# Performance work log

Hardware: AMD Instinct MI355X
Metric: run time of the kernel (lower is better)

Reference implementation:

```python
import jax, jax.numpy as jnp
import numpy as np

B, D_IN, D_Z, N_TRIALS = 4096, 784, 128, 256
T_TEMP = 1.0  # PVAE.t


def setup_inputs() -> dict:
    key = jax.random.key(0)
    ks = jax.random.split(key, 4)
    x = jax.random.normal(ks[0], (B, D_IN), jnp.float32)
    # uniform base samples for reparameterized Exponential(rate) draws
    u = jax.random.uniform(ks[1], (N_TRIALS, B, D_Z), jnp.float32,
                           minval=1e-7, maxval=1.0 - 1e-7)
    W_enc = jax.random.normal(ks[2], (D_IN, D_Z), jnp.float32) * 0.03
    b_enc = jnp.zeros((D_Z,), jnp.float32)
    W_dec = jax.random.normal(ks[3], (D_Z, D_IN), jnp.float32) * 0.08
    b_dec = jnp.zeros((D_IN,), jnp.float32)
    prior = jnp.zeros((1, D_Z), jnp.float32)
    return {"x": x, "u": u, "W_enc": W_enc, "b_enc": b_enc,
            "W_dec": W_dec, "b_dec": b_dec, "prior": prior}


def reference(x, u, W_enc, b_enc, W_dec, b_dec, prior):
    # encoder: du = clamp(Linear(x), max=5)
    du = jnp.minimum(x @ W_enc + b_enc, 5.0)                 # [B, Z]
    # log_rate = clamp(du + clamp(prior, max=5), max=5); rate = exp(.) + 1e-6
    log_rate = jnp.minimum(du + jnp.minimum(prior, 5.0), 5.0)
    rate = jnp.exp(log_rate) + 1e-6                          # [B, Z]
    # exponential race: e ~ Exp(1) via inverse CDF, scaled by 1/rate
    e = -jnp.log1p(-u)                                       # [T, B, Z]
    times = jnp.cumsum(e / rate[None], axis=0)               # prefix sums of arrival times
    # soft indicator (training path, t = 1.0): sigmoid((1 - times) / t)
    indicator = jax.nn.sigmoid((1.0 - times) / T_TEMP)       # [T, B, Z]
    z = jnp.sum(indicator, axis=0)                           # [B, Z] soft Poisson count
    # decoder: sigmoid(Linear(z))
    y = jax.nn.sigmoid(z @ W_dec + b_dec)                    # [B, 784]
    return (du, z, y)
```

## Files before the change

kernel.cpp:

```cpp
#include <hip/hip_runtime.h>
#include <cstdint>
#include <cstddef>

#define LOG2E 1.44269504088896340736f
#define LN2   0.69314718055994530942f

__device__ __forceinline__ float fast_log2(float x) { return __builtin_amdgcn_logf(x); }
__device__ __forceinline__ float fast_exp2(float x) { return __builtin_amdgcn_exp2f(x); }
__device__ __forceinline__ float fast_rcp(float x)  { return __builtin_amdgcn_rcpf(x); }


__global__ __launch_bounds__(256) void enc_kernel(const float* __restrict__ x,
                                                  const float* __restrict__ W,
                                                  const float* __restrict__ bias,
                                                  float* __restrict__ du) {
  __shared__ float xs[16][16];
  __shared__ float ws[16][128];
  const int tid  = threadIdx.x;
  const int row0 = blockIdx.x * 16;
  const int cg   = tid & 31;
  const int rg   = tid >> 5;

  float4 a0 = {0.f, 0.f, 0.f, 0.f};
  float4 a1 = {0.f, 0.f, 0.f, 0.f};

  for (int k0 = 0; k0 < 784; k0 += 16) {
    __syncthreads();
    if (tid < 64) {
      int r = tid >> 2, kc = (tid & 3) * 4;
      *(float4*)&xs[r][kc] = *(const float4*)&x[(size_t)(row0 + r) * 784 + k0 + kc];
    }
#pragma unroll
    for (int j = 0; j < 2; j++) {
      int i = tid + 256 * j;
      int k = i >> 5, c4 = (i & 31) * 4;
      *(float4*)&ws[k][c4] = *(const float4*)&W[(size_t)(k0 + k) * 128 + c4];
    }
    __syncthreads();
#pragma unroll
    for (int k = 0; k < 16; k++) {
      float x0 = xs[rg * 2][k];
      float x1 = xs[rg * 2 + 1][k];
      float4 w = *(const float4*)&ws[k][cg * 4];
      a0.x = fmaf(x0, w.x, a0.x); a0.y = fmaf(x0, w.y, a0.y);
      a0.z = fmaf(x0, w.z, a0.z); a0.w = fmaf(x0, w.w, a0.w);
      a1.x = fmaf(x1, w.x, a1.x); a1.y = fmaf(x1, w.y, a1.y);
      a1.z = fmaf(x1, w.z, a1.z); a1.w = fmaf(x1, w.w, a1.w);
    }
  }

  float4 bb = *(const float4*)&bias[cg * 4];
  float4 r0, r1;
  r0.x = fminf(a0.x + bb.x, 5.f); r0.y = fminf(a0.y + bb.y, 5.f);
  r0.z = fminf(a0.z + bb.z, 5.f); r0.w = fminf(a0.w + bb.w, 5.f);
  r1.x = fminf(a1.x + bb.x, 5.f); r1.y = fminf(a1.y + bb.y, 5.f);
  r1.z = fminf(a1.z + bb.z, 5.f); r1.w = fminf(a1.w + bb.w, 5.f);
  *(float4*)&du[(size_t)(row0 + rg * 2)     * 128 + cg * 4] = r0;
  *(float4*)&du[(size_t)(row0 + rg * 2 + 1) * 128 + cg * 4] = r1;
}

__global__ __launch_bounds__(256) void race_kernel(const float* __restrict__ u,
                                                   const float* __restrict__ du,
                                                   const float* __restrict__ prior,
                                                   float* __restrict__ zout) {
  const int g  = blockIdx.x * 256 + threadIdx.x;
  const int b  = g >> 6;
  const int z0 = (g & 63) * 2;

  const float2 d = *(const float2*)&du[(size_t)b * 128 + z0];
  const float2 p = *(const float2*)&prior[z0];
  const float lr0 = fminf(d.x + fminf(p.x, 5.f), 5.f);
  const float lr1 = fminf(d.y + fminf(p.y, 5.f), 5.f);
  const float rate0 = fast_exp2(lr0 * LOG2E) + 1e-6f;
  const float rate1 = fast_exp2(lr1 * LOG2E) + 1e-6f;
  const float sinv0 = -LN2 / rate0;
  const float sinv1 = -LN2 / rate1;

  float t0 = 0.f, t1 = 0.f, acc0 = 0.f, acc1 = 0.f;
  const float* up = u + (size_t)b * 128 + z0;

#pragma unroll 4
  for (int t = 0; t < 256; t++) {
    float2 uu = *(const float2*)&up[(size_t)t * (4096 * 128)];
    float l0 = fast_log2(1.f - uu.x);
    float l1 = fast_log2(1.f - uu.y);
    t0 = fmaf(l0, sinv0, t0);
    t1 = fmaf(l1, sinv1, t1);
    float e0 = fast_exp2(fmaf(t0, LOG2E, -LOG2E));
    float e1 = fast_exp2(fmaf(t1, LOG2E, -LOG2E));
    acc0 += fast_rcp(1.f + e0);
    acc1 += fast_rcp(1.f + e1);
  }
  float2 r; r.x = acc0; r.y = acc1;
  *(float2*)&zout[(size_t)b * 128 + z0] = r;
}

__global__ __launch_bounds__(256) void dec_kernel(const float* __restrict__ z,
                                                  const float* __restrict__ W,
                                                  const float* __restrict__ bias,
                                                  float* __restrict__ y) {
  __shared__ float zs[8 * 128];
  const int tid = threadIdx.x;
  const int b0  = blockIdx.x * 8;
  *(float4*)&zs[tid * 4] = *(const float4*)&z[(size_t)b0 * 128 + tid * 4];
  __syncthreads();

  for (int col = tid; col < 784; col += 256) {
    float bv = bias[col];
    float acc[8];
#pragma unroll
    for (int i = 0; i < 8; i++) acc[i] = bv;
#pragma unroll 4
    for (int k = 0; k < 128; k++) {
      float w = W[(size_t)k * 784 + col];
#pragma unroll
      for (int i = 0; i < 8; i++) acc[i] = fmaf(zs[i * 128 + k], w, acc[i]);
    }
#pragma unroll
    for (int i = 0; i < 8; i++) {
      float ex = fast_exp2(-acc[i] * LOG2E);
      y[(size_t)(b0 + i) * 784 + col] = fast_rcp(1.f + ex);
    }
  }
}

extern "C" void kernel_launch(void* const* d_in, const int* in_sizes, int n_in,
                              void* d_out, int out_size, void* d_ws, size_t ws_size,
                              hipStream_t stream) {
  const float* x     = (const float*)d_in[0];
  const float* u     = (const float*)d_in[1];
  const float* W_enc = (const float*)d_in[2];
  const float* b_enc = (const float*)d_in[3];
  const float* W_dec = (const float*)d_in[4];
  const float* b_dec = (const float*)d_in[5];
  const float* prior = (const float*)d_in[6];

  float* out = (float*)d_out;
  float* du  = out;
  float* zz  = out + 4096 * 128;
  float* y   = out + 2 * 4096 * 128;

  enc_kernel <<<256,  256, 0, stream>>>(x, W_enc, b_enc, du);
  race_kernel<<<1024, 256, 0, stream>>>(u, du, prior, zz);
  dec_kernel <<<512,  256, 0, stream>>>(zz, W_dec, b_dec, y);
}
```

Baseline: 803.9 us.

## Truncate exponential race once arrival times saturate and widen race lanes to float4

Each race thread now handles four latent dimensions with float4 loads of u, and the launch uses half as many blocks. The trial loop stops per lane once every cumulative arrival time exceeds 18, and exits the wavefront once no lane is active. This skips both the loads of u and the transcendental math for trials whose sigmoid contribution is negligible. The truncation is sound because times only increase, but it adds a small bounded error and makes runtime depend on the rate distribution. The loop also gains a wavefront vote and per-lane branch divergence.

Measured after the change: 789.1 us. No clear change (-1.8%).

```diff
diff --git a/kernel.cpp b/kernel.cpp
--- a/kernel.cpp
+++ b/kernel.cpp
@@ -64,35 +64,53 @@
                                                    const float* __restrict__ prior,
                                                    float* __restrict__ zout) {
   const int g  = blockIdx.x * 256 + threadIdx.x;
-  const int b  = g >> 6;
-  const int z0 = (g & 63) * 2;
+  const int b  = g >> 5;
+  const int z4 = (g & 31) * 4;
 
-  const float2 d = *(const float2*)&du[(size_t)b * 128 + z0];
-  const float2 p = *(const float2*)&prior[z0];
-  const float lr0 = fminf(d.x + fminf(p.x, 5.f), 5.f);
-  const float lr1 = fminf(d.y + fminf(p.y, 5.f), 5.f);
-  const float rate0 = fast_exp2(lr0 * LOG2E) + 1e-6f;
-  const float rate1 = fast_exp2(lr1 * LOG2E) + 1e-6f;
-  const float sinv0 = -LN2 / rate0;
-  const float sinv1 = -LN2 / rate1;
+  const float4 d = *(const float4*)&du[(size_t)b * 128 + z4];
+  const float4 p = *(const float4*)&prior[z4];
 
-  float t0 = 0.f, t1 = 0.f, acc0 = 0.f, acc1 = 0.f;
-  const float* up = u + (size_t)b * 128 + z0;
+  float sinv[4];
+  {
+    const float dd[4] = {d.x, d.y, d.z, d.w};
+    const float pp[4] = {p.x, p.y, p.z, p.w};
+#pragma unroll
+    for (int j = 0; j < 4; j++) {
+      float lr   = fminf(dd[j] + fminf(pp[j], 5.f), 5.f);
+      float rate = fast_exp2(lr * LOG2E) + 1e-6f;
+      sinv[j]    = -LN2 / rate;
+    }
+  }
 
-#pragma unroll 4
-  for (int t = 0; t < 256; t++) {
-    float2 uu = *(const float2*)&up[(size_t)t * (4096 * 128)];
-    float l0 = fast_log2(1.f - uu.x);
-    float l1 = fast_log2(1.f - uu.y);
-    t0 = fmaf(l0, sinv0, t0);
-    t1 = fmaf(l1, sinv1, t1);
-    float e0 = fast_exp2(fmaf(t0, LOG2E, -LOG2E));
-    float e1 = fast_exp2(fmaf(t1, LOG2E, -LOG2E));
-    acc0 += fast_rcp(1.f + e0);
-    acc1 += fast_rcp(1.f + e1);
+  float t[4]   = {0.f, 0.f, 0.f, 0.f};
+  float acc[4] = {0.f, 0.f, 0.f, 0.f};
+  const float* up = u + (size_t)b * 128 + z4;
+  const float TMAX = 18.f;
+
+  for (int tt = 0; tt < 256; tt += 2) {
+    bool act = fminf(fminf(t[0], t[1]), fminf(t[2], t[3])) < TMAX;
+    if (!__any(act)) break;
+    if (act) {
+      float4 ua = *(const float4*)&up[(size_t)tt * (4096 * 128)];
+      float4 ub = *(const float4*)&up[(size_t)(tt + 1) * (4096 * 128)];
+      const float uaj[4] = {ua.x, ua.y, ua.z, ua.w};
+      const float ubj[4] = {ub.x, ub.y, ub.z, ub.w};
+#pragma unroll
+      for (int j = 0; j < 4; j++) {
+        float l = fast_log2(1.f - uaj[j]);
+        t[j] = fmaf(l, sinv[j], t[j]);
+        float e = fast_exp2(fmaf(t[j], LOG2E, -LOG2E));
+        acc[j] += fast_rcp(1.f + e);
+        l = fast_log2(1.f - ubj[j]);
+        t[j] = fmaf(l, sinv[j], t[j]);
+        e = fast_exp2(fmaf(t[j], LOG2E, -LOG2E));
+        acc[j] += fast_rcp(1.f + e);
+      }
+    }
   }
-  float2 r; r.x = acc0; r.y = acc1;
-  *(float2*)&zout[(size_t)b * 128 + z0] = r;
+
+  float4 r; r.x = acc[0]; r.y = acc[1]; r.z = acc[2]; r.w = acc[3];
+  *(float4*)&zout[(size_t)b * 128 + z4] = r;
 }
 
 __global__ __launch_bounds__(256) void dec_kernel(const float* __restrict__ z,
@@ -140,7 +158,7 @@
   float* zz  = out + 4096 * 128;
   float* y   = out + 2 * 4096 * 128;
 
-  enc_kernel <<<256,  256, 0, stream>>>(x, W_enc, b_enc, du);
-  race_kernel<<<1024, 256, 0, stream>>>(u, du, prior, zz);
-  dec_kernel <<<512,  256, 0, stream>>>(zz, W_dec, b_dec, y);
+  enc_kernel <<<256, 256, 0, stream>>>(x, W_enc, b_enc, du);
+  race_kernel<<<512, 256, 0, stream>>>(u, du, prior, zz);
+  dec_kernel <<<512, 256, 0, stream>>>(zz, W_dec, b_dec, y);
 }
```
